# Kernel tuning notes

Hardware: AMD Instinct MI355X
Metric: run time of the kernel (lower is better)

The kernel has to match this reference:

```python
import jax, jax.numpy as jnp
import numpy as np

B, N, F_IN, F, C, E = 8192, 68, 2, 128, 16, 272
EPS = 1e-15


def graph_conv(x, src, dst, W_rel, W_root, b):
    # PyG GraphConv (aggr='add'): out_i = W_rel @ sum_{j->i} x_j + W_root @ x_i + b
    agg = jnp.zeros(x.shape, x.dtype).at[:, dst].add(x[:, src])  # [B,N,Fin]
    return agg @ W_rel.T + x @ W_root.T + b


def setup_inputs() -> dict:
    key = jax.random.key(0)
    ks = jax.random.split(key, 12)
    x = jax.random.normal(ks[0], (B, N, F_IN), jnp.float32)
    edge_index = jax.random.randint(ks[1], (2, E), 0, N, jnp.int32)
    adj = jax.random.uniform(ks[2], (B, N, N), jnp.float32)
    s = jax.random.normal(ks[3], (B, N, C), jnp.float32)
    pos = jax.random.normal(ks[4], (B, N, F_IN), jnp.float32)
    sc = 0.1
    W1_rel = jax.random.normal(ks[5], (F, F_IN), jnp.float32) * sc
    W1_root = jax.random.normal(ks[6], (F, F_IN), jnp.float32) * sc
    b1 = jnp.zeros((F,), jnp.float32)
    W2_rel = jax.random.normal(ks[7], (F, F), jnp.float32) * sc
    W2_root = jax.random.normal(ks[8], (F, F), jnp.float32) * sc
    b2 = jnp.zeros((F,), jnp.float32)
    W3_rel = jax.random.normal(ks[9], (F, F), jnp.float32) * sc
    W3_root = jax.random.normal(ks[10], (F, F), jnp.float32) * sc
    b3 = jnp.zeros((F,), jnp.float32)
    return dict(x=x, edge_index=edge_index, adj=adj, s=s, pos=pos,
                W1_rel=W1_rel, W1_root=W1_root, b1=b1,
                W2_rel=W2_rel, W2_root=W2_root, b2=b2,
                W3_rel=W3_rel, W3_root=W3_root, b3=b3)


def reference(x, edge_index, adj, s, pos,
              W1_rel, W1_root, b1, W2_rel, W2_root, b2, W3_rel, W3_root, b3):
    src, dst = edge_index[0], edge_index[1]
    h = jax.nn.relu(graph_conv(x, src, dst, W1_rel, W1_root, b1))
    h = jax.nn.relu(graph_conv(h, src, dst, W2_rel, W2_root, b2))
    h = jax.nn.relu(graph_conv(h, src, dst, W3_rel, W3_root, b3))  # [B,N,F]
    # dense_diff_pool
    s_sm = jax.nn.softmax(s, axis=-1)                       # [B,N,C]
    out = jnp.einsum('bnc,bnf->bcf', s_sm, h)               # [B,C,F]
    out_adj = jnp.einsum('bnc,bnm,bmk->bck', s_sm, adj, s_sm)  # [B,C,C]
    diff = adj - jnp.einsum('bnc,bmc->bnm', s_sm, s_sm)
    link_loss = jnp.sqrt(jnp.sum(diff * diff)) / adj.size
    ent_loss = jnp.mean(jnp.sum(-s_sm * jnp.log(s_sm + EPS), axis=-1))
    return (out, out_adj, link_loss, ent_loss, pos)
```

## Files before the change

### kernel.cpp

```cpp
#include <hip/hip_runtime.h>
#include <math.h>

#define B_   8192
#define N_   68
#define FIN  2
#define F_   128
#define C_   16
#define E_   272

#define OUT_OFF  0
#define ADJ_OFF  (B_*C_*F_)
#define LINK_IDX (ADJ_OFF + B_*C_*C_)
#define ENT_IDX  (LINK_IDX + 1)
#define POS_OFF  (ENT_IDX + 1)

#define WS_CSR_OFF  131072
#define WS_W_OFF    133120
#define WS_AG_OFF   264192

typedef __attribute__((ext_vector_type(8))) short bf16x8;
typedef __attribute__((ext_vector_type(4))) float f32x4;

#define SWZ256(r, cb) (((r) * 256) + ((cb) ^ (((r) & 7) << 4)))
#define SWZ512(r, cb) (((r) * 512) + ((cb) ^ (((r) & 7) << 4)))
#define SWZH(r, cb)   (((r) * 192) + ((cb) ^ (((r) & 3) << 4)))
#define MFMA16(a, bb, c) __builtin_amdgcn_mfma_f32_16x16x32_bf16((a), (bb), (c), 0, 0, 0)

__device__ __forceinline__ short bf16_rne(float x) {
  unsigned u = __builtin_bit_cast(unsigned, x);
  u += 0x7FFFu + ((u >> 16) & 1u);
  return (short)(u >> 16);
}
__device__ __forceinline__ short4 pack4(f32x4 v) {
  short4 s;
  s.x = bf16_rne(v[0]); s.y = bf16_rne(v[1]); s.z = bf16_rne(v[2]); s.w = bf16_rne(v[3]);
  return s;
}

__global__ void prep_kernel(const int* __restrict__ edge_index,
                            const float* __restrict__ W2r, const float* __restrict__ W2o,
                            const float* __restrict__ W3r, const float* __restrict__ W3o,
                            int* __restrict__ csr, short* __restrict__ wcat,
                            short* __restrict__ agw) {
  int gid = blockIdx.x * blockDim.x + threadIdx.x;
  for (int e = gid; e < 2 * F_ * 256; e += gridDim.x * blockDim.x) {
    int layer = e >> 15, idx = e & 32767;
    int j = idx >> 8, k = idx & 255;
    const float* Wr = layer ? W3r : W2r;
    const float* Wo = layer ? W3o : W2o;
    float v = (k < F_) ? Wr[j * F_ + k] : Wo[j * F_ + (k - F_)];
    wcat[e] = bf16_rne(v);
  }
  __shared__ unsigned short cnt[80 * 128];
  __shared__ int src_s[E_], dst_s[E_], cc[N_], offs[N_ + 1];
  if (blockIdx.x == 0) {
    int t = threadIdx.x;
    for (int i = t; i < 80 * 128; i += blockDim.x) cnt[i] = 0;
    for (int e = t; e < E_; e += blockDim.x) { src_s[e] = edge_index[e]; dst_s[e] = edge_index[E_ + e]; }
    for (int n = t; n < N_; n += blockDim.x) cc[n] = 0;
    __syncthreads();
    if (t == 0) {
      for (int e = 0; e < E_; ++e) { cnt[dst_s[e] * 128 + src_s[e]]++; cc[dst_s[e]]++; }
      offs[0] = 0;
      for (int n = 0; n < N_; ++n) offs[n + 1] = offs[n] + cc[n];
      for (int n = 0; n < N_; ++n) cc[n] = offs[n];
      for (int e = 0; e < E_; ++e) { int d = dst_s[e]; csr[N_ + 1 + cc[d]++] = src_s[e]; }
      for (int n = 0; n <= N_; ++n) csr[n] = offs[n];
    }
    __syncthreads();
    for (int i = t; i < 80 * 128; i += blockDim.x) agw[i] = bf16_rne((float)cnt[i]);
  }
}

__launch_bounds__(512, 4)
__global__ void layers_kernel(
    const float* __restrict__ x, const float* __restrict__ s,
    const float* __restrict__ W1r, const float* __restrict__ W1o, const float* __restrict__ b1,
    const float* __restrict__ b2f, const float* __restrict__ b3f,
    const short* __restrict__ wcat, const short* __restrict__ agw,
    float* __restrict__ out, const int* __restrict__ csr)
{
  __shared__ __align__(16) short Hn[80 * 256];
  __shared__ __align__(16) short HT[128 * 96];
  __shared__ __align__(16) short ssmT[16 * 128];
  __shared__ float xb[N_ * FIN], axb[N_ * FIN];
  __shared__ int offs[N_ + 1], srcs[E_];

  const int b = blockIdx.x, tid = threadIdx.x;
  const int lane = tid & 63, wave = tid >> 6;
  const int l15 = lane & 15, lg = lane >> 4;
  const int j0 = wave * 16;

  for (int i = tid; i < N_ + 1; i += 512) offs[i] = csr[i];
  for (int i = tid; i < E_; i += 512) srcs[i] = csr[N_ + 1 + i];
  for (int i = tid; i < N_ * FIN; i += 512) xb[i] = x[(size_t)b * N_ * FIN + i];
  {
    int4 zz; zz.x = 0; zz.y = 0; zz.z = 0; zz.w = 0;
    for (int i = tid; i < 384; i += 512) {
      int r = 68 + (i >> 5), cb = (i & 31) * 16;
      *(int4*)((char*)Hn + SWZ512(r, cb)) = zz;
    }
    long long z8 = 0;
    for (int i = tid; i < 128 * 7; i += 512) {
      int r = i / 7, cb = 136 + (i % 7) * 8;
      *(long long*)((char*)HT + SWZH(r, cb)) = z8;
    }
    for (int i = tid; i < 16 * 7; i += 512) {
      int r = i / 7, cb = 136 + (i % 7) * 8;
      *(long long*)((char*)ssmT + SWZ256(r, cb)) = z8;
    }
  }
  if (tid < N_) {
    const float* srow = &s[((size_t)b * N_ + tid) * C_];
    float sv[16];
    float mx = -1e30f;
#pragma unroll
    for (int c = 0; c < 16; ++c) { sv[c] = srow[c]; mx = fmaxf(mx, sv[c]); }
    float sum = 0.f;
#pragma unroll
    for (int c = 0; c < 16; ++c) { sv[c] = expf(sv[c] - mx); sum += sv[c]; }
    float inv = 1.f / sum;
#pragma unroll
    for (int c = 0; c < 16; ++c)
      *(short*)((char*)ssmT + SWZ256(c, tid * 2)) = bf16_rne(sv[c] * inv);
  }
  __syncthreads();

  if (tid < N_) {
    float a0 = 0, a1 = 0;
    for (int e = offs[tid]; e < offs[tid + 1]; ++e) {
      int sr = srcs[e];
      a0 += xb[sr * 2]; a1 += xb[sr * 2 + 1];
    }
    axb[tid * 2] = a0; axb[tid * 2 + 1] = a1;
  }
  __syncthreads();

  {
    int f4 = (tid & 31) * 4;
    float4 R0 = *(const float4*)&W1r[f4 * 2], R1 = *(const float4*)&W1r[f4 * 2 + 4];
    float4 O0 = *(const float4*)&W1o[f4 * 2], O1 = *(const float4*)&W1o[f4 * 2 + 4];
    float4 Bv = *(const float4*)&b1[f4];
#pragma unroll
    for (int p = 0; p < 5; ++p) {
      int n = p * 16 + (tid >> 5);
      if (n < N_) {
        float a0 = axb[n * 2], a1 = axb[n * 2 + 1], x0 = xb[n * 2], x1 = xb[n * 2 + 1];
        f32x4 v;
        v[0] = fmaxf(a0 * R0.x + a1 * R0.y + x0 * O0.x + x1 * O0.y + Bv.x, 0.f);
        v[1] = fmaxf(a0 * R0.z + a1 * R0.w + x0 * O0.z + x1 * O0.w + Bv.y, 0.f);
        v[2] = fmaxf(a0 * R1.x + a1 * R1.y + x0 * O1.x + x1 * O1.y + Bv.z, 0.f);
        v[3] = fmaxf(a0 * R1.z + a1 * R1.w + x0 * O1.z + x1 * O1.w + Bv.w, 0.f);
        *(short4*)((char*)Hn + SWZ512(n, 256 + f4 * 2)) = pack4(v);
      }
    }
  }
  {
    int f = tid >> 2, nq = tid & 3;
    float wr0 = W1r[f * 2], wr1 = W1r[f * 2 + 1];
    float wo0 = W1o[f * 2], wo1 = W1o[f * 2 + 1];
    float bv = b1[f];
#pragma unroll
    for (int p = 0; p < 5; ++p) {
      int n0 = p * 16 + nq * 4;
      if (n0 < N_) {
        f32x4 Aa = *(const f32x4*)&axb[n0 * 2], Ab = *(const f32x4*)&axb[n0 * 2 + 4];
        f32x4 Xa = *(const f32x4*)&xb[n0 * 2],  Xb = *(const f32x4*)&xb[n0 * 2 + 4];
        f32x4 v;
        v[0] = fmaxf(Aa[0] * wr0 + Aa[1] * wr1 + Xa[0] * wo0 + Xa[1] * wo1 + bv, 0.f);
        v[1] = fmaxf(Aa[2] * wr0 + Aa[3] * wr1 + Xa[2] * wo0 + Xa[3] * wo1 + bv, 0.f);
        v[2] = fmaxf(Ab[0] * wr0 + Ab[1] * wr1 + Xb[0] * wo0 + Xb[1] * wo1 + bv, 0.f);
        v[3] = fmaxf(Ab[2] * wr0 + Ab[3] * wr1 + Xb[2] * wo0 + Xb[3] * wo1 + bv, 0.f);
        *(short4*)((char*)HT + SWZH(f, n0 * 2)) = pack4(v);
      }
    }
  }

  {
    bf16x8 hA[3];
#pragma unroll
    for (int ks = 0; ks < 3; ++ks)
      hA[ks] = *(const bf16x8*)((const char*)HT + SWZH(j0 + l15, ks * 64 + 16 * lg));
#pragma unroll
    for (int nt = 0; nt < 5; ++nt) {
      f32x4 acc = {0.f, 0.f, 0.f, 0.f};
#pragma unroll
      for (int ks = 0; ks < 3; ++ks)
        acc = MFMA16(hA[ks], *(const bf16x8*)(agw + (nt * 16 + l15) * 128 + ks * 32 + lg * 8), acc);
      *(short4*)((char*)Hn + SWZ512(nt * 16 + l15, (j0 + lg * 4) * 2)) = pack4(acc);
    }
  }
  __syncthreads();

  {
    f32x4 accL[5];
    bf16x8 Bw[8];
#pragma unroll
    for (int ks = 0; ks < 8; ++ks)
      Bw[ks] = *(const bf16x8*)(wcat + (j0 + l15) * 256 + ks * 32 + 8 * lg);
#pragma unroll
    for (int mt = 0; mt < 5; ++mt) {
      f32x4 acc = {0.f, 0.f, 0.f, 0.f};
#pragma unroll
      for (int ks = 0; ks < 8; ++ks)
        acc = MFMA16(*(const bf16x8*)((const char*)Hn + SWZ512(mt * 16 + l15, ks * 64 + 16 * lg)), Bw[ks], acc);
      accL[mt] = acc;
    }
    __syncthreads();
    float bv = b2f[j0 + l15];
#pragma unroll
    for (int mt = 0; mt < 5; ++mt) {
      f32x4 v;
#pragma unroll
      for (int r = 0; r < 4; ++r) {
        float t = accL[mt][r] + bv;
        v[r] = t > 0.f ? t : 0.f;
      }
      short4 p = pack4(v);
      *(short*)((char*)Hn + SWZ512(mt * 16 + lg * 4 + 0, 256 + (j0 + l15) * 2)) = p.x;
      *(short*)((char*)Hn + SWZ512(mt * 16 + lg * 4 + 1, 256 + (j0 + l15) * 2)) = p.y;
      *(short*)((char*)Hn + SWZ512(mt * 16 + lg * 4 + 2, 256 + (j0 + l15) * 2)) = p.z;
      *(short*)((char*)Hn + SWZ512(mt * 16 + lg * 4 + 3, 256 + (j0 + l15) * 2)) = p.w;
      *(short4*)((char*)HT + SWZH(j0 + l15, (mt * 16 + lg * 4) * 2)) = p;
    }
  }

  {
    bf16x8 hA[3];
#pragma unroll
    for (int ks = 0; ks < 3; ++ks)
      hA[ks] = *(const bf16x8*)((const char*)HT + SWZH(j0 + l15, ks * 64 + 16 * lg));
#pragma unroll
    for (int nt = 0; nt < 5; ++nt) {
      f32x4 acc = {0.f, 0.f, 0.f, 0.f};
#pragma unroll
      for (int ks = 0; ks < 3; ++ks)
        acc = MFMA16(hA[ks], *(const bf16x8*)(agw + (nt * 16 + l15) * 128 + ks * 32 + lg * 8), acc);
      *(short4*)((char*)Hn + SWZ512(nt * 16 + l15, (j0 + lg * 4) * 2)) = pack4(acc);
    }
  }
  __syncthreads();

  {
    bf16x8 Bw[8];
#pragma unroll
    for (int ks = 0; ks < 8; ++ks)
      Bw[ks] = *(const bf16x8*)(wcat + 32768 + (j0 + l15) * 256 + ks * 32 + 8 * lg);
    float bv = b3f[j0 + l15];
#pragma unroll
    for (int mt = 0; mt < 5; ++mt) {
      f32x4 acc = {0.f, 0.f, 0.f, 0.f};
#pragma unroll
      for (int ks = 0; ks < 8; ++ks)
        acc = MFMA16(*(const bf16x8*)((const char*)Hn + SWZ512(mt * 16 + l15, ks * 64 + 16 * lg)), Bw[ks], acc);
      f32x4 v;
#pragma unroll
      for (int r = 0; r < 4; ++r) {
        float t = acc[r] + bv;
        v[r] = t > 0.f ? t : 0.f;
      }
      *(short4*)((char*)HT + SWZH(j0 + l15, (mt * 16 + lg * 4) * 2)) = pack4(v);
    }
  }

  {
    f32x4 acc = {0.f, 0.f, 0.f, 0.f};
#pragma unroll
    for (int ks = 0; ks < 3; ++ks)
      acc = MFMA16(*(const bf16x8*)((const char*)HT + SWZH(j0 + l15, ks * 64 + 16 * lg)),
                   *(const bf16x8*)((const char*)ssmT + SWZ256(l15, ks * 64 + 16 * lg)), acc);
    float4 st; st.x = acc[0]; st.y = acc[1]; st.z = acc[2]; st.w = acc[3];
    *(float4*)&out[OUT_OFF + (size_t)b * C_ * F_ + l15 * F_ + j0 + lg * 4] = st;
  }
}

__launch_bounds__(512, 4)
__global__ void pool_kernel(
    const float* __restrict__ adj, const float* __restrict__ s, const float* __restrict__ pos,
    float* __restrict__ out, double* __restrict__ partials)
{
  __shared__ __align__(16) short AdjB[80 * 128];
  __shared__ __align__(16) short ssmT[16 * 128];
  __shared__ __align__(16) short TT[16 * 128];
  __shared__ double red[16];

  const int b = blockIdx.x, tid = threadIdx.x;
  const int lane = tid & 63, wave = tid >> 6;
  const int l15 = lane & 15, lg = lane >> 4;

  {
    long long z8 = 0;
    for (int i = tid; i < 1200; i += 512) {
      int r = i / 15, cb = 136 + (i % 15) * 8;
      *(long long*)((char*)AdjB + SWZ256(r, cb)) = z8;
    }
    for (int i = tid; i < 204; i += 512) {
      int r = 68 + i / 17, cb = (i % 17) * 8;
      *(long long*)((char*)AdjB + SWZ256(r, cb)) = z8;
    }
    for (int i = tid; i < 16 * 7; i += 512) {
      int r = i / 7, cb = 136 + (i % 7) * 8;
      *(long long*)((char*)ssmT + SWZ256(r, cb)) = z8;
      *(long long*)((char*)TT + SWZ256(r, cb)) = z8;
    }
  }
  float sadj2 = 0.f;
  const float* adjb = &adj[(size_t)b * N_ * N_];
  for (int q = tid; q < N_ * N_; q += 512) {
    int n = q / N_, m = q - n * N_;
    float v = adjb[q];
    sadj2 += v * v;
    *(short*)((char*)AdjB + SWZ256(n, m * 2)) = bf16_rne(v);
  }
  float entPart = 0.f;
  if (tid < N_) {
    const float* srow = &s[((size_t)b * N_ + tid) * C_];
    float sv[16], ev[16];
    float mx = -1e30f;
#pragma unroll
    for (int c = 0; c < 16; ++c) { sv[c] = srow[c]; mx = fmaxf(mx, sv[c]); }
    float sum = 0.f;
#pragma unroll
    for (int c = 0; c < 16; ++c) { ev[c] = expf(sv[c] - mx); sum += ev[c]; }
    float inv = 1.f / sum, ps = 0.f;
#pragma unroll
    for (int c = 0; c < 16; ++c) {
      float pv = ev[c] * inv;
      ps += pv * sv[c];
      *(short*)((char*)ssmT + SWZ256(c, tid * 2)) = bf16_rne(pv);
    }
    entPart = (mx + logf(sum)) - ps;
  }
  for (int i = tid; i < N_ * FIN; i += 512)
    out[POS_OFF + (size_t)b * N_ * FIN + i] = pos[(size_t)b * N_ * FIN + i];
  __syncthreads();

  float g2Part = 0.f;
  if (wave < 5) {
    f32x4 acc = {0.f, 0.f, 0.f, 0.f};
#pragma unroll
    for (int ks = 0; ks < 3; ++ks)
      acc = MFMA16(*(const bf16x8*)((const char*)AdjB + SWZ256(wave * 16 + l15, ks * 64 + 16 * lg)),
                   *(const bf16x8*)((const char*)ssmT + SWZ256(l15, ks * 64 + 16 * lg)), acc);
#pragma unroll
    for (int r = 0; r < 4; ++r) {
      int n = wave * 16 + lg * 4 + r;
      if (n < N_) *(short*)((char*)TT + SWZ256(l15, n * 2)) = bf16_rne(acc[r]);
    }
  } else if (wave == 5) {
    f32x4 acc = {0.f, 0.f, 0.f, 0.f};
#pragma unroll
    for (int ks = 0; ks < 3; ++ks) {
      bf16x8 a = *(const bf16x8*)((const char*)ssmT + SWZ256(l15, ks * 64 + 16 * lg));
      acc = MFMA16(a, a, acc);
    }
#pragma unroll
    for (int r = 0; r < 4; ++r) g2Part += acc[r] * acc[r];
  }
  __syncthreads();

  float trPart = 0.f;
  if (wave == 0) {
    f32x4 acc = {0.f, 0.f, 0.f, 0.f};
#pragma unroll
    for (int ks = 0; ks < 3; ++ks)
      acc = MFMA16(*(const bf16x8*)((const char*)ssmT + SWZ256(l15, ks * 64 + 16 * lg)),
                   *(const bf16x8*)((const char*)TT + SWZ256(l15, ks * 64 + 16 * lg)), acc);
#pragma unroll
    for (int r = 0; r < 4; ++r) {
      int c = lg * 4 + r;
      out[ADJ_OFF + (size_t)b * 256 + c * 16 + l15] = acc[r];
      if (c == l15) trPart += acc[r];
    }
  }

  double lk = (double)sadj2 - 2.0 * (double)trPart + (double)g2Part;
  double en = (double)entPart;
  for (int o = 32; o > 0; o >>= 1) { lk += __shfl_down(lk, o); en += __shfl_down(en, o); }
  if ((tid & 63) == 0) { red[wave] = lk; red[8 + wave] = en; }
  __syncthreads();
  if (tid == 0) {
    double L = 0, En = 0;
    for (int w = 0; w < 8; ++w) { L += red[w]; En += red[8 + w]; }
    partials[2 * b] = L;
    partials[2 * b + 1] = En;
  }
}

__global__ void finalize_kernel(const double* __restrict__ partials, float* __restrict__ out) {
  __shared__ double red[16];
  int tid = threadIdx.x;
  double L = 0, En = 0;
  for (int i = tid; i < B_; i += 512) { L += partials[2 * i]; En += partials[2 * i + 1]; }
  for (int o = 32; o > 0; o >>= 1) { L += __shfl_down(L, o); En += __shfl_down(En, o); }
  if ((tid & 63) == 0) { red[tid >> 6] = L; red[8 + (tid >> 6)] = En; }
  __syncthreads();
  if (tid == 0) {
    double Ls = 0, Es = 0;
    for (int w = 0; w < 8; ++w) { Ls += red[w]; Es += red[8 + w]; }
    out[LINK_IDX] = (float)(sqrt(Ls) / (double)((size_t)B_ * N_ * N_));
    out[ENT_IDX] = (float)(Es / (double)((size_t)B_ * N_));
  }
}

extern "C" void kernel_launch(void* const* d_in, const int* in_sizes, int n_in,
                              void* d_out, int out_size, void* d_ws, size_t ws_size,
                              hipStream_t stream) {
  const float* x   = (const float*)d_in[0];
  const int*   ei  = (const int*)d_in[1];
  const float* adj = (const float*)d_in[2];
  const float* s   = (const float*)d_in[3];
  const float* pos = (const float*)d_in[4];
  const float* W1r = (const float*)d_in[5];
  const float* W1o = (const float*)d_in[6];
  const float* b1  = (const float*)d_in[7];
  const float* W2r = (const float*)d_in[8];
  const float* W2o = (const float*)d_in[9];
  const float* b2  = (const float*)d_in[10];
  const float* W3r = (const float*)d_in[11];
  const float* W3o = (const float*)d_in[12];
  const float* b3  = (const float*)d_in[13];

  float* out = (float*)d_out;
  double* partials = (double*)d_ws;
  int* csr = (int*)((char*)d_ws + WS_CSR_OFF);
  short* wcat = (short*)((char*)d_ws + WS_W_OFF);
  short* agw  = (short*)((char*)d_ws + WS_AG_OFF);

  prep_kernel<<<65, 512, 0, stream>>>(ei, W2r, W2o, W3r, W3o, csr, wcat, agw);
  layers_kernel<<<B_, 512, 0, stream>>>(x, s, W1r, W1o, b1, b2, b3, wcat, agw, out, csr);
  pool_kernel<<<B_, 512, 0, stream>>>(adj, s, pos, out, partials);
  finalize_kernel<<<1, 512, 0, stream>>>(partials, out);
}
```

Before: 520.9 us.

## Reorder GraphConv as transform-then-aggregate with ping-pong node-major buffers

Each GraphConv layer now first multiplies node features by W_rel and W_root (two MFMA chains sharing the same H operand), then aggregates the W_rel product through the adjacency-count matrix, instead of aggregating first and then doing a K=256 GEMM on the concatenated [agg|h] buffer. This removes the transposed HT copy, the extra sync and scalar scattered writes, and lets layer 1 write only the node-major buffer, ping-ponging halves of Hn between layers. The cost is an extra bf16 rounding of the intermediate U=H·W_relᵀ and more live accumulator registers (10 f32x4 plus 8 weight fragments) under the 512-thread, 4-block launch bound.

```diff
diff --git a/kernel.cpp b/kernel.cpp
--- a/kernel.cpp
+++ b/kernel.cpp
@@ -72,6 +72,63 @@
   }
 }
 
+__device__ __forceinline__ void layer_mfma(short* Hn, short* UT,
+    const short* __restrict__ wl, const float* __restrict__ bias,
+    const short* __restrict__ agw,
+    int hinB, int houtB, int outT, int l15, int lg, int j0)
+{
+  bf16x8 Ar[4], Ao[4];
+#pragma unroll
+  for (int ks = 0; ks < 4; ++ks) {
+    Ar[ks] = *(const bf16x8*)(wl + (j0 + l15) * 256 + ks * 32 + 8 * lg);
+    Ao[ks] = *(const bf16x8*)(wl + (j0 + l15) * 256 + 128 + ks * 32 + 8 * lg);
+  }
+  f32x4 U0 = {0,0,0,0}, U1 = {0,0,0,0}, U2 = {0,0,0,0}, U3 = {0,0,0,0}, U4 = {0,0,0,0};
+  f32x4 V0 = {0,0,0,0}, V1 = {0,0,0,0}, V2 = {0,0,0,0}, V3 = {0,0,0,0}, V4 = {0,0,0,0};
+#define G1_(UN, VN, NT) do { \
+  _Pragma("unroll") \
+  for (int ks = 0; ks < 4; ++ks) { \
+    bf16x8 b_ = *(const bf16x8*)((const char*)Hn + SWZ512((NT) * 16 + l15, hinB + ks * 64 + 16 * lg)); \
+    UN = MFMA16(Ar[ks], b_, UN); \
+    VN = MFMA16(Ao[ks], b_, VN); \
+  } \
+} while (0)
+  G1_(U0, V0, 0); G1_(U1, V1, 1); G1_(U2, V2, 2); G1_(U3, V3, 3); G1_(U4, V4, 4);
+#undef G1_
+#define UTW_(UN, NT) do { \
+  _Pragma("unroll") \
+  for (int q = 0; q < 4; ++q) \
+    *(short*)((char*)UT + SWZH(j0 + lg * 4 + q, ((NT) * 16 + l15) * 2)) = bf16_rne(UN[q]); \
+} while (0)
+  UTW_(U0, 0); UTW_(U1, 1); UTW_(U2, 2); UTW_(U3, 3); UTW_(U4, 4);
+#undef UTW_
+  bf16x8 aU[3];
+#pragma unroll
+  for (int ks = 0; ks < 3; ++ks)
+    aU[ks] = *(const bf16x8*)((const char*)UT + SWZH(j0 + l15, ks * 64 + 16 * lg));
+  float4 bv = *(const float4*)&bias[j0 + lg * 4];
+#define G2_(VN, NT) do { \
+  f32x4 acc = {0.f, 0.f, 0.f, 0.f}; \
+  _Pragma("unroll") \
+  for (int ks = 0; ks < 3; ++ks) \
+    acc = MFMA16(aU[ks], *(const bf16x8*)(agw + ((NT) * 16 + l15) * 128 + ks * 32 + lg * 8), acc); \
+  f32x4 v_; \
+  v_[0] = fmaxf(acc[0] + VN[0] + bv.x, 0.f); \
+  v_[1] = fmaxf(acc[1] + VN[1] + bv.y, 0.f); \
+  v_[2] = fmaxf(acc[2] + VN[2] + bv.z, 0.f); \
+  v_[3] = fmaxf(acc[3] + VN[3] + bv.w, 0.f); \
+  if (!outT) { \
+    *(short4*)((char*)Hn + SWZ512((NT) * 16 + l15, houtB + (j0 + lg * 4) * 2)) = pack4(v_); \
+  } else { \
+    _Pragma("unroll") \
+    for (int q = 0; q < 4; ++q) \
+      *(short*)((char*)UT + SWZH(j0 + lg * 4 + q, ((NT) * 16 + l15) * 2)) = bf16_rne(v_[q]); \
+  } \
+} while (0)
+  G2_(V0, 0); G2_(V1, 1); G2_(V2, 2); G2_(V3, 3); G2_(V4, 4);
+#undef G2_
+}
+
 __launch_bounds__(512, 4)
 __global__ void layers_kernel(
     const float* __restrict__ x, const float* __restrict__ s,
@@ -81,7 +138,7 @@
     float* __restrict__ out, const int* __restrict__ csr)
 {
   __shared__ __align__(16) short Hn[80 * 256];
-  __shared__ __align__(16) short HT[128 * 96];
+  __shared__ __align__(16) short UT[128 * 96];
   __shared__ __align__(16) short ssmT[16 * 128];
   __shared__ float xb[N_ * FIN], axb[N_ * FIN];
   __shared__ int offs[N_ + 1], srcs[E_];
@@ -101,9 +158,9 @@
       *(int4*)((char*)Hn + SWZ512(r, cb)) = zz;
     }
     long long z8 = 0;
-    for (int i = tid; i < 128 * 7; i += 512) {
-      int r = i / 7, cb = 136 + (i % 7) * 8;
-      *(long long*)((char*)HT + SWZH(r, cb)) = z8;
+    for (int i = tid; i < 128 * 2; i += 512) {
+      int r = i >> 1, cb = 160 + (i & 1) * 16;
+      *(int4*)((char*)UT + SWZH(r, cb)) = zz;
     }
     for (int i = tid; i < 16 * 7; i += 512) {
       int r = i / 7, cb = 136 + (i % 7) * 8;
@@ -151,123 +208,22 @@
         v[1] = fmaxf(a0 * R0.z + a1 * R0.w + x0 * O0.z + x1 * O0.w + Bv.y, 0.f);
         v[2] = fmaxf(a0 * R1.x + a1 * R1.y + x0 * O1.x + x1 * O1.y + Bv.z, 0.f);
         v[3] = fmaxf(a0 * R1.z + a1 * R1.w + x0 * O1.z + x1 * O1.w + Bv.w, 0.f);
-        *(short4*)((char*)Hn + SWZ512(n, 256 + f4 * 2)) = pack4(v);
+        *(short4*)((char*)Hn + SWZ512(n, f4 * 2)) = pack4(v);
       }
     }
   }
-  {
-    int f = tid >> 2, nq = tid & 3;
-    float wr0 = W1r[f * 2], wr1 = W1r[f * 2 + 1];
-    float wo0 = W1o[f * 2], wo1 = W1o[f * 2 + 1];
-    float bv = b1[f];
-#pragma unroll
-    for (int p = 0; p < 5; ++p) {
-      int n0 = p * 16 + nq * 4;
-      if (n0 < N_) {
-        f32x4 Aa = *(const f32x4*)&axb[n0 * 2], Ab = *(const f32x4*)&axb[n0 * 2 + 4];
-        f32x4 Xa = *(const f32x4*)&xb[n0 * 2],  Xb = *(const f32x4*)&xb[n0 * 2 + 4];
-        f32x4 v;
-        v[0] = fmaxf(Aa[0] * wr0 + Aa[1] * wr1 + Xa[0] * wo0 + Xa[1] * wo1 + bv, 0.f);
-        v[1] = fmaxf(Aa[2] * wr0 + Aa[3] * wr1 + Xa[2] * wo0 + Xa[3] * wo1 + bv, 0.f);
-        v[2] = fmaxf(Ab[0] * wr0 + Ab[1] * wr1 + Xb[0] * wo0 + Xb[1] * wo1 + bv, 0.f);
-        v[3] = fmaxf(Ab[2] * wr0 + Ab[3] * wr1 + Xb[2] * wo0 + Xb[3] * wo1 + bv, 0.f);
-        *(short4*)((char*)HT + SWZH(f, n0 * 2)) = pack4(v);
-      }
-    }
-  }
-
-  {
-    bf16x8 hA[3];
-#pragma unroll
-    for (int ks = 0; ks < 3; ++ks)
-      hA[ks] = *(const bf16x8*)((const char*)HT + SWZH(j0 + l15, ks * 64 + 16 * lg));
-#pragma unroll
-    for (int nt = 0; nt < 5; ++nt) {
-      f32x4 acc = {0.f, 0.f, 0.f, 0.f};
-#pragma unroll
-      for (int ks = 0; ks < 3; ++ks)
-        acc = MFMA16(hA[ks], *(const bf16x8*)(agw + (nt * 16 + l15) * 128 + ks * 32 + lg * 8), acc);
-      *(short4*)((char*)Hn + SWZ512(nt * 16 + l15, (j0 + lg * 4) * 2)) = pack4(acc);
-    }
-  }
-  __syncthreads();
-
-  {
-    f32x4 accL[5];
-    bf16x8 Bw[8];
-#pragma unroll
-    for (int ks = 0; ks < 8; ++ks)
-      Bw[ks] = *(const bf16x8*)(wcat + (j0 + l15) * 256 + ks * 32 + 8 * lg);
-#pragma unroll
-    for (int mt = 0; mt < 5; ++mt) {
-      f32x4 acc = {0.f, 0.f, 0.f, 0.f};
-#pragma unroll
-      for (int ks = 0; ks < 8; ++ks)
-        acc = MFMA16(*(const bf16x8*)((const char*)Hn + SWZ512(mt * 16 + l15, ks * 64 + 16 * lg)), Bw[ks], acc);
-      accL[mt] = acc;
-    }
-    __syncthreads();
-    float bv = b2f[j0 + l15];
-#pragma unroll
-    for (int mt = 0; mt < 5; ++mt) {
-      f32x4 v;
-#pragma unroll
-      for (int r = 0; r < 4; ++r) {
-        float t = accL[mt][r] + bv;
-        v[r] = t > 0.f ? t : 0.f;
-      }
-      short4 p = pack4(v);
-      *(short*)((char*)Hn + SWZ512(mt * 16 + lg * 4 + 0, 256 + (j0 + l15) * 2)) = p.x;
-      *(short*)((char*)Hn + SWZ512(mt * 16 + lg * 4 + 1, 256 + (j0 + l15) * 2)) = p.y;
-      *(short*)((char*)Hn + SWZ512(mt * 16 + lg * 4 + 2, 256 + (j0 + l15) * 2)) = p.z;
-      *(short*)((char*)Hn + SWZ512(mt * 16 + lg * 4 + 3, 256 + (j0 + l15) * 2)) = p.w;
-      *(short4*)((char*)HT + SWZH(j0 + l15, (mt * 16 + lg * 4) * 2)) = p;
-    }
-  }
-
-  {
-    bf16x8 hA[3];
-#pragma unroll
-    for (int ks = 0; ks < 3; ++ks)
-      hA[ks] = *(const bf16x8*)((const char*)HT + SWZH(j0 + l15, ks * 64 + 16 * lg));
-#pragma unroll
-    for (int nt = 0; nt < 5; ++nt) {
-      f32x4 acc = {0.f, 0.f, 0.f, 0.f};
-#pragma unroll
-      for (int ks = 0; ks < 3; ++ks)
-        acc = MFMA16(hA[ks], *(const bf16x8*)(agw + (nt * 16 + l15) * 128 + ks * 32 + lg * 8), acc);
-      *(short4*)((char*)Hn + SWZ512(nt * 16 + l15, (j0 + lg * 4) * 2)) = pack4(acc);
-    }
-  }
-  __syncthreads();
-
-  {
-    bf16x8 Bw[8];
-#pragma unroll
-    for (int ks = 0; ks < 8; ++ks)
-      Bw[ks] = *(const bf16x8*)(wcat + 32768 + (j0 + l15) * 256 + ks * 32 + 8 * lg);
-    float bv = b3f[j0 + l15];
-#pragma unroll
-    for (int mt = 0; mt < 5; ++mt) {
-      f32x4 acc = {0.f, 0.f, 0.f, 0.f};
-#pragma unroll
-      for (int ks = 0; ks < 8; ++ks)
-        acc = MFMA16(*(const bf16x8*)((const char*)Hn + SWZ512(mt * 16 + l15, ks * 64 + 16 * lg)), Bw[ks], acc);
-      f32x4 v;
-#pragma unroll
-      for (int r = 0; r < 4; ++r) {
-        float t = acc[r] + bv;
-        v[r] = t > 0.f ? t : 0.f;
-      }
-      *(short4*)((char*)HT + SWZH(j0 + l15, (mt * 16 + lg * 4) * 2)) = pack4(v);
-    }
-  }
+  __syncthreads();
+
+  layer_mfma(Hn, UT, wcat, b2f, agw, 0, 256, 0, l15, lg, j0);
+  __syncthreads();
+
+  layer_mfma(Hn, UT, wcat + 32768, b3f, agw, 256, 0, 1, l15, lg, j0);
 
   {
     f32x4 acc = {0.f, 0.f, 0.f, 0.f};
 #pragma unroll
     for (int ks = 0; ks < 3; ++ks)
-      acc = MFMA16(*(const bf16x8*)((const char*)HT + SWZH(j0 + l15, ks * 64 + 16 * lg)),
+      acc = MFMA16(*(const bf16x8*)((const char*)UT + SWZH(j0 + l15, ks * 64 + 16 * lg)),
                    *(const bf16x8*)((const char*)ssmT + SWZ256(l15, ks * 64 + 16 * lg)), acc);
     float4 st; st.x = acc[0]; st.y = acc[1]; st.z = acc[2]; st.w = acc[3];
     *(float4*)&out[OUT_OFF + (size_t)b * C_ * F_ + l15 * F_ + j0 + lg * 4] = st;
```

Result: faster. 485.1 us (-6.9%).
